# Kernel optimization log

Hardware: AMD Instinct MI355X
Metric: run time of the kernel (lower is better)

Reference implementation:

```python
import jax, jax.numpy as jnp
import numpy as np

T = 300  # windowsize = windowstep(50) * windowmul(6)
D_IN = 39
H1, H2 = 35, 30
FC1, FC2, OUT = 50, 40, 2


def _lstm_layer(x_tbd, W, b, H):
    """TF LSTMCell: gates ordered i, j, f, o; forget_bias=1.0; tanh activation.
    x_tbd: [T, B, D]; W: [D+H, 4H]; b: [4H]. Returns hidden states [T, B, H]."""
    B = x_tbd.shape[1]
    h0 = jnp.zeros((B, H), x_tbd.dtype)
    c0 = jnp.zeros((B, H), x_tbd.dtype)

    def step(carry, xt):
        h, c = carry
        z = jnp.concatenate([xt, h], axis=-1) @ W + b  # [B, 4H]
        i, j, f, o = jnp.split(z, 4, axis=-1)
        c = jax.nn.sigmoid(f + 1.0) * c + jax.nn.sigmoid(i) * jnp.tanh(j)
        h = jax.nn.sigmoid(o) * jnp.tanh(c)
        return (h, c), h

    _, hs = jax.lax.scan(step, (h0, c0), x_tbd)
    return hs


def _stack(x_tbd, W1, b1, W2, b2):
    h1 = _lstm_layer(x_tbd, W1, b1, H1)
    return _lstm_layer(h1, W2, b2, H2)


def setup_inputs() -> dict:
    key = jax.random.key(0)
    ks = jax.random.split(key, 16)
    B = 4096
    s = lambda fan_in: 1.0 / np.sqrt(fan_in)

    def mat(k, shape):
        return jax.random.normal(k, shape, jnp.float32) * s(shape[0])

    return {
        "x": jax.random.normal(ks[0], (B, T, D_IN), jnp.float32),
        "fw_W1": mat(ks[1], (D_IN + H1, 4 * H1)), "fw_b1": jnp.zeros((4 * H1,), jnp.float32),
        "fw_W2": mat(ks[2], (H1 + H2, 4 * H2)), "fw_b2": jnp.zeros((4 * H2,), jnp.float32),
        "bw_W1": mat(ks[3], (D_IN + H1, 4 * H1)), "bw_b1": jnp.zeros((4 * H1,), jnp.float32),
        "bw_W2": mat(ks[4], (H1 + H2, 4 * H2)), "bw_b2": jnp.zeros((4 * H2,), jnp.float32),
        "W_fc1": mat(ks[5], (2 * H2, FC1)), "b_fc1": jnp.zeros((FC1,), jnp.float32),
        "W_fc2": mat(ks[6], (FC1, FC2)), "b_fc2": jnp.zeros((FC2,), jnp.float32),
        "W_out": mat(ks[7], (FC2, OUT)), "b_out": jnp.zeros((OUT,), jnp.float32),
    }


def reference(x, fw_W1, fw_b1, fw_W2, fw_b2, bw_W1, bw_b1, bw_W2, bw_b2,
              W_fc1, b_fc1, W_fc2, b_fc2, W_out, b_out):
    x_tbd = jnp.transpose(x, (1, 0, 2))  # [T, B, D]
    h_fw = _stack(x_tbd, fw_W1, fw_b1, fw_W2, fw_b2)               # [T, B, H2]
    h_bw = _stack(x_tbd[::-1], bw_W1, bw_b1, bw_W2, bw_b2)[::-1]   # [T, B, H2]
    h = jnp.concatenate([h_fw, h_bw], axis=-1)  # [T, B, 2*H2]
    h = jnp.transpose(h, (1, 0, 2))             # [B, T, 60]
    h = jax.nn.relu(h @ W_fc1 + b_fc1)
    h = jax.nn.relu(h @ W_fc2 + b_fc2)
    logits = h @ W_out + b_out                  # [B, T, 2]
    return logits
```

## Files before the change

### kernel.cpp

```cpp
#include <hip/hip_runtime.h>


#define T_STEPS 300
#define DIN 39
#define H1 35
#define H2 30
#define BATCH 4096
#define FC1N 50
#define FC2N 40

#define AP_STR 104

typedef _Float16 f16;
typedef _Float16 half8 __attribute__((ext_vector_type(8)));
typedef float floatx4 __attribute__((ext_vector_type(4)));

__device__ __forceinline__ float sigf(float x) {
    return __builtin_amdgcn_rcpf(1.0f + __expf(-x));
}
__device__ __forceinline__ float sig_tanh(float a, float b) {
    float bc = fminf(b, 30.0f);
    float ea = __expf(-a);
    float E  = __expf(2.0f * bc);
    return (E - 1.0f) * __builtin_amdgcn_rcpf((1.0f + ea) * (E + 1.0f));
}

__global__ void wprep_kernel(const float* __restrict__ fw1, const float* __restrict__ bw1,
                             const float* __restrict__ fw2, const float* __restrict__ bw2,
                             f16* __restrict__ bp) {
    int frag = blockIdx.x;
    int lane = threadIdx.x;
    int dir = frag / 60;
    int rem = frag % 60;
    int layer = (rem < 36) ? 0 : 1;
    int r2 = (layer == 0) ? rem : rem - 36;
    int ug = r2 / 12, g = (r2 % 12) / 3, c = r2 % 3;
    int u = ug * 16 + (lane & 15);
    const float* W = (layer == 0) ? (dir ? bw1 : fw1) : (dir ? bw2 : fw2);
    for (int j = 0; j < 8; ++j) {
        int k = c * 32 + (lane >> 4) * 8 + j;
        float v = 0.0f;
        if (layer == 0) {
            if (u < H1) {
                int kr = (k < 39) ? k : ((k >= 40 && k < 75) ? k - 1 : -1);
                if (kr >= 0) v = W[kr * (4 * H1) + g * H1 + u];
            }
        } else {
            if (u < H2 && k < 65) v = W[k * (4 * H2) + g * H2 + u];
        }
        bp[(size_t)frag * 512 + lane * 8 + j] = (f16)v;
    }
}

__global__ void fcwprep_kernel(const float* __restrict__ Wf1, const float* __restrict__ Wf2,
                               const float* __restrict__ Wo, f16* __restrict__ fcp) {
    int f = blockIdx.x;
    int lane = threadIdx.x;
    int lm = lane & 15, oct = lane >> 4;
    for (int j = 0; j < 8; ++j) {
        float v = 0.0f;
        if (f < 8) {
            int tile = f >> 1, chunk = f & 1;
            int n = tile * 16 + lm;
            int kl = chunk * 32 + oct * 8 + j;
            int krow = (kl < 30) ? kl : ((kl >= 32 && kl < 62) ? kl - 2 : -1);
            if (n < FC1N && krow >= 0) v = Wf1[krow * FC1N + n];
        } else if (f < 14) {
            int g = f - 8, tile = g >> 1, chunk = g & 1;
            int n = tile * 16 + lm;
            int k = chunk * 32 + oct * 8 + j;
            if (n < FC2N && k < FC1N) v = Wf2[k * FC2N + n];
        } else {
            int chunk = f - 14;
            int k = chunk * 32 + oct * 8 + j;
            if (lm < 2 && k < FC2N) v = Wo[k * 2 + lm];
        }
        fcp[(size_t)f * 512 + lane * 8 + j] = (f16)v;
    }
}

__global__ __launch_bounds__(320, 3) void lstm_fused(
    const float* __restrict__ x, const f16* __restrict__ bp,
    const float* __restrict__ fb1, const float* __restrict__ bb1,
    const float* __restrict__ fb2, const float* __restrict__ bb2,
    f16* __restrict__ h2s)
{
    __shared__ f16 pan1[2][16 * AP_STR];
    __shared__ f16 pan2[2][16 * AP_STR];

    const int tid = threadIdx.x;
    const int b0  = blockIdx.x * 16;
    const int dir = blockIdx.y;
    const int wv   = tid >> 6;
    const int lane = tid & 63;
    const int lm = lane & 15, oct = lane >> 4;
    const bool isL2 = (wv >= 3);
    const int ug = isL2 ? (wv - 3) : wv;
    const int u  = ug * 16 + lm;
    const int Hn = isL2 ? H2 : H1;
    const float* bias = isL2 ? (dir ? bb2 : fb2) : (dir ? bb1 : fb1);
    const int fragbase = dir * 60 + (isL2 ? 36 : 0) + ug * 12;

    half8 bf[4][3];
    #pragma unroll
    for (int g = 0; g < 4; ++g)
        #pragma unroll
        for (int c = 0; c < 3; ++c)
            bf[g][c] = *(const half8*)(bp + (size_t)(fragbase + g * 3 + c) * 512 + lane * 8);

    float zb[4];
    #pragma unroll
    for (int g = 0; g < 4; ++g)
        zb[g] = (u < Hn) ? bias[g * Hn + u] : 0.f;
    float cst[4] = {0.f, 0.f, 0.f, 0.f};

    f16* h2p = h2s + ((size_t)(dir * BATCH + b0 + oct * 4) * T_STEPS
                      + (dir ? (T_STEPS - 1) : 0)) * 32 + u;
    const int h2step = dir ? -32 : 32;

    for (int idx = tid; idx < 16 * AP_STR; idx += 320) {
        pan1[0][idx] = (f16)0.f; pan1[1][idx] = (f16)0.f;
        pan2[0][idx] = (f16)0.f; pan2[1][idx] = (f16)0.f;
    }
    __syncthreads();

    const int sr = tid / 10, sq = tid % 10;
    float xv[4] = {0.f, 0.f, 0.f, 0.f};
    if (tid < 160) {
        int t0 = dir ? (T_STEPS - 1) : 0;
        const float* p0 = x + ((size_t)(b0 + sr) * T_STEPS + t0) * DIN;
        union { f16 h[4]; uint2 u; } pk;
        #pragma unroll
        for (int i = 0; i < 4; ++i) { int k = sq * 4 + i; pk.h[i] = (k < DIN) ? (f16)p0[k] : (f16)0.f; }
        *(uint2*)(&pan1[0][sr * AP_STR + sq * 4]) = pk.u;
        int t1 = dir ? (T_STEPS - 2) : 1;
        const float* p1 = x + ((size_t)(b0 + sr) * T_STEPS + t1) * DIN;
        #pragma unroll
        for (int i = 0; i < 4; ++i) { int k = sq * 4 + i; xv[i] = (k < DIN) ? p1[k] : 0.f; }
    }
    __syncthreads();

    const int arow = lm * AP_STR + oct * 8;

    if (!isL2) {
        floatx4 C[4];
        #pragma unroll
        for (int g = 0; g < 4; ++g) C[g] = (floatx4){zb[g], zb[g], zb[g], zb[g]};
        half8 a0 = *(const half8*)(&pan1[0][arow]);
        half8 a1 = *(const half8*)(&pan1[0][arow + 32]);
        half8 a2 = *(const half8*)(&pan1[0][arow + 64]);
        #pragma unroll
        for (int g = 0; g < 4; ++g) {
            C[g] = __builtin_amdgcn_mfma_f32_16x16x32_f16(a0, bf[g][0], C[g], 0, 0, 0);
            C[g] = __builtin_amdgcn_mfma_f32_16x16x32_f16(a1, bf[g][1], C[g], 0, 0, 0);
            C[g] = __builtin_amdgcn_mfma_f32_16x16x32_f16(a2, bf[g][2], C[g], 0, 0, 0);
        }
        #pragma unroll
        for (int r = 0; r < 4; ++r) {
            float cc = sigf(C[2][r] + 1.0f) * cst[r] + sig_tanh(C[0][r], C[1][r]);
            cst[r] = cc;
            float hh = sig_tanh(C[3][r], cc);
            if (u < H1) {
                int row = oct * 4 + r;
                f16 hv = (f16)hh;
                pan1[1][row * AP_STR + 40 + u] = hv;
                pan2[1][row * AP_STR + u] = hv;
            }
        }
    }
    const float* px = x + ((size_t)(b0 + sr) * T_STEPS
                           + (dir ? (T_STEPS - 4) : 3)) * DIN + sq * 4;
    const int xstep = dir ? -DIN : DIN;
    if (tid < 160) {
        union { f16 h[4]; uint2 u; } pk;
        #pragma unroll
        for (int i = 0; i < 4; ++i) pk.h[i] = (f16)xv[i];
        *(uint2*)(&pan1[1][sr * AP_STR + sq * 4]) = pk.u;
        int t2 = dir ? (T_STEPS - 3) : 2;
        const float* p2 = x + ((size_t)(b0 + sr) * T_STEPS + t2) * DIN;
        #pragma unroll
        for (int i = 0; i < 4; ++i) { int k = sq * 4 + i; xv[i] = (k < DIN) ? p2[k] : 0.f; }
    }
    __syncthreads();

    for (int s = 0; s < T_STEPS; ++s) {
        const int p = 1 - (s & 1);

        float xn[4] = {0.f, 0.f, 0.f, 0.f};
        if (tid < 160) {
            #pragma unroll
            for (int i = 0; i < 4; ++i) { int k = sq * 4 + i; xn[i] = (k < DIN) ? px[i] : 0.f; }
        }
        if (s < T_STEPS - 4) px += xstep;

        const f16* ap = isL2 ? &pan2[p][0] : &pan1[p][0];
        floatx4 C[4];
        #pragma unroll
        for (int g = 0; g < 4; ++g) C[g] = (floatx4){zb[g], zb[g], zb[g], zb[g]};
        {
            half8 a0 = *(const half8*)(ap + arow);
            half8 a1 = *(const half8*)(ap + arow + 32);
            half8 a2 = *(const half8*)(ap + arow + 64);
            #pragma unroll
            for (int g = 0; g < 4; ++g) {
                C[g] = __builtin_amdgcn_mfma_f32_16x16x32_f16(a0, bf[g][0], C[g], 0, 0, 0);
                C[g] = __builtin_amdgcn_mfma_f32_16x16x32_f16(a1, bf[g][1], C[g], 0, 0, 0);
                C[g] = __builtin_amdgcn_mfma_f32_16x16x32_f16(a2, bf[g][2], C[g], 0, 0, 0);
            }
        }

        f16* w1 = &pan1[1 - p][0];
        f16* w2 = &pan2[1 - p][0];
        if (!isL2) {
            #pragma unroll
            for (int r = 0; r < 4; ++r) {
                float cc = sigf(C[2][r] + 1.0f) * cst[r] + sig_tanh(C[0][r], C[1][r]);
                cst[r] = cc;
                float hh = sig_tanh(C[3][r], cc);
                if (u < H1) {
                    int row = oct * 4 + r;
                    f16 hv = (f16)hh;
                    w1[row * AP_STR + 40 + u] = hv;
                    w2[row * AP_STR + u] = hv;
                }
            }
        } else {
            #pragma unroll
            for (int r = 0; r < 4; ++r) {
                float dd = sigf(C[2][r] + 1.0f) * cst[r] + sig_tanh(C[0][r], C[1][r]);
                cst[r] = dd;
                float gg = sig_tanh(C[3][r], dd);
                if (u < H2) {
                    int row = oct * 4 + r;
                    f16 gv = (f16)gg;
                    w2[row * AP_STR + 35 + u] = gv;
                    h2p[(size_t)r * T_STEPS * 32] = gv;
                }
            }
        }
        h2p += h2step;

        if (tid < 160) {
            union { f16 h[4]; uint2 u; } pk;
            #pragma unroll
            for (int i = 0; i < 4; ++i) pk.h[i] = (f16)xv[i];
            *(uint2*)(&pan1[1 - p][sr * AP_STR + sq * 4]) = pk.u;
            #pragma unroll
            for (int i = 0; i < 4; ++i) xv[i] = xn[i];
        }
        __syncthreads();
    }
}

__global__ __launch_bounds__(256, 4) void fc_kernel(
    const f16* __restrict__ h2s, const f16* __restrict__ fcp,
    const float* __restrict__ bf1, const float* __restrict__ bf2,
    const float* __restrict__ bo, float* __restrict__ out)
{
    __shared__ f16 apf[4][64 * 72];
    const int tid = threadIdx.x;
    const int wv = tid >> 6, lane = tid & 63;
    const int lm = lane & 15, oct = lane >> 4;
    f16* ap = apf[wv];

    half8 wf[16];
    #pragma unroll
    for (int f = 0; f < 16; ++f)
        wf[f] = *(const half8*)(fcp + (size_t)f * 512 + lane * 8);

    const int ar = lm * 72 + oct * 8;
    const int row = lane >> 2, seg = lane & 3;
    const size_t base = (size_t)blockIdx.x * 256 + wv * 64;

    uint4 vf[4], vb[4];
    #pragma unroll
    for (int g = 0; g < 4; ++g) {
        const size_t r0 = base + g * 16 + row;
        vf[g] = *(const uint4*)(h2s + r0 * 32 + seg * 8);
        vb[g] = *(const uint4*)(h2s + ((size_t)BATCH * T_STEPS + r0) * 32 + seg * 8);
    }
    #pragma unroll
    for (int g = 0; g < 4; ++g) {
        *(uint4*)(ap + (g * 16 + row) * 72 + seg * 8) = vf[g];
        *(uint4*)(ap + (g * 16 + row) * 72 + 32 + seg * 8) = vb[g];
    }

    #pragma unroll
    for (int g = 0; g < 4; ++g) {
        f16* agp = ap + g * 16 * 72;
        half8 a0 = *(const half8*)(agp + ar);
        half8 a1 = *(const half8*)(agp + ar + 32);
        floatx4 C[4];
        #pragma unroll
        for (int t = 0; t < 4; ++t) {
            int col = t * 16 + lm;
            float b = (col < FC1N) ? bf1[col] : 0.f;
            C[t] = (floatx4){b, b, b, b};
            C[t] = __builtin_amdgcn_mfma_f32_16x16x32_f16(a0, wf[t * 2 + 0], C[t], 0, 0, 0);
            C[t] = __builtin_amdgcn_mfma_f32_16x16x32_f16(a1, wf[t * 2 + 1], C[t], 0, 0, 0);
        }
        #pragma unroll
        for (int t = 0; t < 4; ++t) {
            int col = t * 16 + lm;
            #pragma unroll
            for (int r = 0; r < 4; ++r)
                agp[(oct * 4 + r) * 72 + col] = (f16)fmaxf(C[t][r], 0.f);
        }
    }

    #pragma unroll
    for (int g = 0; g < 4; ++g) {
        f16* agp = ap + g * 16 * 72;
        half8 a0 = *(const half8*)(agp + ar);
        half8 a1 = *(const half8*)(agp + ar + 32);
        floatx4 D[3];
        #pragma unroll
        for (int t = 0; t < 3; ++t) {
            int col = t * 16 + lm;
            float b = (col < FC2N) ? bf2[col] : 0.f;
            D[t] = (floatx4){b, b, b, b};
            D[t] = __builtin_amdgcn_mfma_f32_16x16x32_f16(a0, wf[8 + t * 2 + 0], D[t], 0, 0, 0);
            D[t] = __builtin_amdgcn_mfma_f32_16x16x32_f16(a1, wf[8 + t * 2 + 1], D[t], 0, 0, 0);
        }
        #pragma unroll
        for (int t = 0; t < 3; ++t) {
            int col = t * 16 + lm;
            #pragma unroll
            for (int r = 0; r < 4; ++r)
                agp[(oct * 4 + r) * 72 + col] = (f16)fmaxf(D[t][r], 0.f);
        }
    }

    #pragma unroll
    for (int g = 0; g < 4; ++g) {
        f16* agp = ap + g * 16 * 72;
        half8 a0 = *(const half8*)(agp + ar);
        half8 a1 = *(const half8*)(agp + ar + 32);
        float b = (lm < 2) ? bo[lm] : 0.f;
        floatx4 E = (floatx4){b, b, b, b};
        E = __builtin_amdgcn_mfma_f32_16x16x32_f16(a0, wf[14], E, 0, 0, 0);
        E = __builtin_amdgcn_mfma_f32_16x16x32_f16(a1, wf[15], E, 0, 0, 0);
        if (lm < 2) {
            const size_t rid0 = base + g * 16;
            #pragma unroll
            for (int r = 0; r < 4; ++r)
                out[(rid0 + oct * 4 + r) * 2 + lm] = E[r];
        }
    }
}

extern "C" void kernel_launch(void* const* d_in, const int* in_sizes, int n_in,
                              void* d_out, int out_size, void* d_ws, size_t ws_size,
                              hipStream_t stream) {
    const float* x     = (const float*)d_in[0];
    const float* fw_W1 = (const float*)d_in[1];
    const float* fw_b1 = (const float*)d_in[2];
    const float* fw_W2 = (const float*)d_in[3];
    const float* fw_b2 = (const float*)d_in[4];
    const float* bw_W1 = (const float*)d_in[5];
    const float* bw_b1 = (const float*)d_in[6];
    const float* bw_W2 = (const float*)d_in[7];
    const float* bw_b2 = (const float*)d_in[8];
    const float* Wf1   = (const float*)d_in[9];
    const float* bf1   = (const float*)d_in[10];
    const float* Wf2   = (const float*)d_in[11];
    const float* bf2   = (const float*)d_in[12];
    const float* Wo    = (const float*)d_in[13];
    const float* bo    = (const float*)d_in[14];
    float* outp = (float*)d_out;

    f16* h2s = (f16*)d_ws;
    f16* bp  = h2s + (size_t)2 * BATCH * T_STEPS * 32;
    f16* fcp = bp + (size_t)120 * 512;

    wprep_kernel<<<120, 64, 0, stream>>>(fw_W1, bw_W1, fw_W2, bw_W2, bp);
    fcwprep_kernel<<<16, 64, 0, stream>>>(Wf1, Wf2, Wo, fcp);

    dim3 gl(BATCH / 16, 2);
    lstm_fused<<<gl, 320, 0, stream>>>(x, bp, fw_b1, bw_b1, fw_b2, bw_b2, h2s);

    fc_kernel<<<(BATCH * T_STEPS) / 256, 256, 0, stream>>>(
        h2s, fcp, bf1, bf2, bo, outp);
}
```

Before: 665.9 us.

## Merge LSTM layer panels into one shared buffer and stream FC inputs from registers

Layer-1 and layer-2 A-panels are combined into a single shared panel per parity buffer. Layer 2 now reads a window offset by 40, so each layer-1 hidden state is written to LDS once instead of twice and shared memory per block shrinks. The FC kernel loads the fwd/bwd hidden fragments directly from global memory into MFMA A registers, prefetching the next 16-row group, so the LDS staging copy goes away. FC1 weights are repacked to match the new layout. Risks: the padding columns of the panel must stay zero, and layer-2 stores are no longer guarded by u<H2, so the padded lanes must produce values that are harmless.

```diff
diff --git a/kernel.cpp b/kernel.cpp
--- a/kernel.cpp
+++ b/kernel.cpp
@@ -9,7 +9,7 @@
 #define FC1N 50
 #define FC2N 40
 
-#define AP_STR 104
+#define PAN_STR 136
 
 typedef _Float16 f16;
 typedef _Float16 half8 __attribute__((ext_vector_type(8)));
@@ -62,9 +62,8 @@
         if (f < 8) {
             int tile = f >> 1, chunk = f & 1;
             int n = tile * 16 + lm;
-            int kl = chunk * 32 + oct * 8 + j;
-            int krow = (kl < 30) ? kl : ((kl >= 32 && kl < 62) ? kl - 2 : -1);
-            if (n < FC1N && krow >= 0) v = Wf1[krow * FC1N + n];
+            int kl = oct * 8 + j;
+            if (n < FC1N && kl < 30) v = Wf1[(chunk * 30 + kl) * FC1N + n];
         } else if (f < 14) {
             int g = f - 8, tile = g >> 1, chunk = g & 1;
             int n = tile * 16 + lm;
@@ -85,8 +84,7 @@
     const float* __restrict__ fb2, const float* __restrict__ bb2,
     f16* __restrict__ h2s)
 {
-    __shared__ f16 pan1[2][16 * AP_STR];
-    __shared__ f16 pan2[2][16 * AP_STR];
+    __shared__ f16 pan[2][16 * PAN_STR];
 
     const int tid = threadIdx.x;
     const int b0  = blockIdx.x * 16;
@@ -118,9 +116,8 @@
                       + (dir ? (T_STEPS - 1) : 0)) * 32 + u;
     const int h2step = dir ? -32 : 32;
 
-    for (int idx = tid; idx < 16 * AP_STR; idx += 320) {
-        pan1[0][idx] = (f16)0.f; pan1[1][idx] = (f16)0.f;
-        pan2[0][idx] = (f16)0.f; pan2[1][idx] = (f16)0.f;
+    for (int idx = tid; idx < 16 * PAN_STR; idx += 320) {
+        pan[0][idx] = (f16)0.f; pan[1][idx] = (f16)0.f;
     }
     __syncthreads();
 
@@ -132,7 +129,7 @@
         union { f16 h[4]; uint2 u; } pk;
         #pragma unroll
         for (int i = 0; i < 4; ++i) { int k = sq * 4 + i; pk.h[i] = (k < DIN) ? (f16)p0[k] : (f16)0.f; }
-        *(uint2*)(&pan1[0][sr * AP_STR + sq * 4]) = pk.u;
+        *(uint2*)(&pan[0][sr * PAN_STR + sq * 4]) = pk.u;
         int t1 = dir ? (T_STEPS - 2) : 1;
         const float* p1 = x + ((size_t)(b0 + sr) * T_STEPS + t1) * DIN;
         #pragma unroll
@@ -140,15 +137,15 @@
     }
     __syncthreads();
 
-    const int arow = lm * AP_STR + oct * 8;
+    const int arow = lm * PAN_STR + oct * 8 + (isL2 ? 40 : 0);
 
     if (!isL2) {
         floatx4 C[4];
         #pragma unroll
         for (int g = 0; g < 4; ++g) C[g] = (floatx4){zb[g], zb[g], zb[g], zb[g]};
-        half8 a0 = *(const half8*)(&pan1[0][arow]);
-        half8 a1 = *(const half8*)(&pan1[0][arow + 32]);
-        half8 a2 = *(const half8*)(&pan1[0][arow + 64]);
+        half8 a0 = *(const half8*)(&pan[0][arow]);
+        half8 a1 = *(const half8*)(&pan[0][arow + 32]);
+        half8 a2 = *(const half8*)(&pan[0][arow + 64]);
         #pragma unroll
         for (int g = 0; g < 4; ++g) {
             C[g] = __builtin_amdgcn_mfma_f32_16x16x32_f16(a0, bf[g][0], C[g], 0, 0, 0);
@@ -162,9 +159,7 @@
             float hh = sig_tanh(C[3][r], cc);
             if (u < H1) {
                 int row = oct * 4 + r;
-                f16 hv = (f16)hh;
-                pan1[1][row * AP_STR + 40 + u] = hv;
-                pan2[1][row * AP_STR + u] = hv;
+                pan[1][row * PAN_STR + 40 + u] = (f16)hh;
             }
         }
     }
@@ -175,7 +170,7 @@
         union { f16 h[4]; uint2 u; } pk;
         #pragma unroll
         for (int i = 0; i < 4; ++i) pk.h[i] = (f16)xv[i];
-        *(uint2*)(&pan1[1][sr * AP_STR + sq * 4]) = pk.u;
+        *(uint2*)(&pan[1][sr * PAN_STR + sq * 4]) = pk.u;
         int t2 = dir ? (T_STEPS - 3) : 2;
         const float* p2 = x + ((size_t)(b0 + sr) * T_STEPS + t2) * DIN;
         #pragma unroll
@@ -193,7 +188,7 @@
         }
         if (s < T_STEPS - 4) px += xstep;
 
-        const f16* ap = isL2 ? &pan2[p][0] : &pan1[p][0];
+        const f16* ap = &pan[p][0];
         floatx4 C[4];
         #pragma unroll
         for (int g = 0; g < 4; ++g) C[g] = (floatx4){zb[g], zb[g], zb[g], zb[g]};
@@ -209,8 +204,7 @@
             }
         }
 
-        f16* w1 = &pan1[1 - p][0];
-        f16* w2 = &pan2[1 - p][0];
+        f16* w = &pan[1 - p][0];
         if (!isL2) {
             #pragma unroll
             for (int r = 0; r < 4; ++r) {
@@ -219,9 +213,7 @@
                 float hh = sig_tanh(C[3][r], cc);
                 if (u < H1) {
                     int row = oct * 4 + r;
-                    f16 hv = (f16)hh;
-                    w1[row * AP_STR + 40 + u] = hv;
-                    w2[row * AP_STR + u] = hv;
+                    w[row * PAN_STR + 40 + u] = (f16)hh;
                 }
             }
         } else {
@@ -230,12 +222,10 @@
                 float dd = sigf(C[2][r] + 1.0f) * cst[r] + sig_tanh(C[0][r], C[1][r]);
                 cst[r] = dd;
                 float gg = sig_tanh(C[3][r], dd);
-                if (u < H2) {
-                    int row = oct * 4 + r;
-                    f16 gv = (f16)gg;
-                    w2[row * AP_STR + 35 + u] = gv;
-                    h2p[(size_t)r * T_STEPS * 32] = gv;
-                }
+                int row = oct * 4 + r;
+                f16 gv = (f16)gg;
+                w[row * PAN_STR + 75 + u] = gv;
+                h2p[(size_t)r * T_STEPS * 32] = gv;
             }
         }
         h2p += h2step;
@@ -244,7 +234,7 @@
             union { f16 h[4]; uint2 u; } pk;
             #pragma unroll
             for (int i = 0; i < 4; ++i) pk.h[i] = (f16)xv[i];
-            *(uint2*)(&pan1[1 - p][sr * AP_STR + sq * 4]) = pk.u;
+            *(uint2*)(&pan[1 - p][sr * PAN_STR + sq * 4]) = pk.u;
             #pragma unroll
             for (int i = 0; i < 4; ++i) xv[i] = xn[i];
         }
@@ -252,16 +242,22 @@
     }
 }
 
-__global__ __launch_bounds__(256, 4) void fc_kernel(
+__global__ __launch_bounds__(256) void fc_kernel(
     const f16* __restrict__ h2s, const f16* __restrict__ fcp,
     const float* __restrict__ bf1, const float* __restrict__ bf2,
     const float* __restrict__ bo, float* __restrict__ out)
 {
-    __shared__ f16 apf[4][64 * 72];
+    __shared__ f16 apf[4][2][16 * 72];
     const int tid = threadIdx.x;
     const int wv = tid >> 6, lane = tid & 63;
     const int lm = lane & 15, oct = lane >> 4;
-    f16* ap = apf[wv];
+    f16* pa = &apf[wv][0][0];
+    f16* pb = &apf[wv][1][0];
+
+    {
+        uint* z = (uint*)pa;
+        for (int i = lane; i < 1152; i += 64) z[i] = 0u;
+    }
 
     half8 wf[16];
     #pragma unroll
@@ -269,27 +265,23 @@
         wf[f] = *(const half8*)(fcp + (size_t)f * 512 + lane * 8);
 
     const int ar = lm * 72 + oct * 8;
-    const int row = lane >> 2, seg = lane & 3;
     const size_t base = (size_t)blockIdx.x * 256 + wv * 64;
-
-    uint4 vf[4], vb[4];
-    #pragma unroll
-    for (int g = 0; g < 4; ++g) {
-        const size_t r0 = base + g * 16 + row;
-        vf[g] = *(const uint4*)(h2s + r0 * 32 + seg * 8);
-        vb[g] = *(const uint4*)(h2s + ((size_t)BATCH * T_STEPS + r0) * 32 + seg * 8);
-    }
-    #pragma unroll
-    for (int g = 0; g < 4; ++g) {
-        *(uint4*)(ap + (g * 16 + row) * 72 + seg * 8) = vf[g];
-        *(uint4*)(ap + (g * 16 + row) * 72 + 32 + seg * 8) = vb[g];
-    }
-
-    #pragma unroll
-    for (int g = 0; g < 4; ++g) {
-        f16* agp = ap + g * 16 * 72;
-        half8 a0 = *(const half8*)(agp + ar);
-        half8 a1 = *(const half8*)(agp + ar + 32);
+    const size_t bwoff = (size_t)BATCH * T_STEPS * 32;
+
+    union U8 { uint4 u; half8 h; };
+    const f16* gp = h2s + (base + lm) * 32 + oct * 8;
+    U8 va, vb;
+    va.u = *(const uint4*)gp;
+    vb.u = *(const uint4*)(gp + bwoff);
+
+    for (int it = 0; it < 4; ++it) {
+        half8 a0 = va.h, a1 = vb.h;
+        if (it < 3) {
+            const f16* gn = gp + (size_t)(it + 1) * 16 * 32;
+            va.u = *(const uint4*)gn;
+            vb.u = *(const uint4*)(gn + bwoff);
+        }
+
         floatx4 C[4];
         #pragma unroll
         for (int t = 0; t < 4; ++t) {
@@ -304,44 +296,36 @@
             int col = t * 16 + lm;
             #pragma unroll
             for (int r = 0; r < 4; ++r)
-                agp[(oct * 4 + r) * 72 + col] = (f16)fmaxf(C[t][r], 0.f);
-        }
-    }
-
-    #pragma unroll
-    for (int g = 0; g < 4; ++g) {
-        f16* agp = ap + g * 16 * 72;
-        half8 a0 = *(const half8*)(agp + ar);
-        half8 a1 = *(const half8*)(agp + ar + 32);
+                pa[(oct * 4 + r) * 72 + col] = (f16)fmaxf(C[t][r], 0.f);
+        }
+
+        half8 b0 = *(const half8*)(pa + ar);
+        half8 b1 = *(const half8*)(pa + ar + 32);
         floatx4 D[3];
         #pragma unroll
         for (int t = 0; t < 3; ++t) {
             int col = t * 16 + lm;
             float b = (col < FC2N) ? bf2[col] : 0.f;
             D[t] = (floatx4){b, b, b, b};
-            D[t] = __builtin_amdgcn_mfma_f32_16x16x32_f16(a0, wf[8 + t * 2 + 0], D[t], 0, 0, 0);
-            D[t] = __builtin_amdgcn_mfma_f32_16x16x32_f16(a1, wf[8 + t * 2 + 1], D[t], 0, 0, 0);
+            D[t] = __builtin_amdgcn_mfma_f32_16x16x32_f16(b0, wf[8 + t * 2 + 0], D[t], 0, 0, 0);
+            D[t] = __builtin_amdgcn_mfma_f32_16x16x32_f16(b1, wf[8 + t * 2 + 1], D[t], 0, 0, 0);
         }
         #pragma unroll
         for (int t = 0; t < 3; ++t) {
             int col = t * 16 + lm;
             #pragma unroll
             for (int r = 0; r < 4; ++r)
-                agp[(oct * 4 + r) * 72 + col] = (f16)fmaxf(D[t][r], 0.f);
-        }
-    }
-
-    #pragma unroll
-    for (int g = 0; g < 4; ++g) {
-        f16* agp = ap + g * 16 * 72;
-        half8 a0 = *(const half8*)(agp + ar);
-        half8 a1 = *(const half8*)(agp + ar + 32);
+                pb[(oct * 4 + r) * 72 + col] = (f16)fmaxf(D[t][r], 0.f);
+        }
+
+        half8 c0 = *(const half8*)(pb + ar);
+        half8 c1 = *(const half8*)(pb + ar + 32);
         float b = (lm < 2) ? bo[lm] : 0.f;
         floatx4 E = (floatx4){b, b, b, b};
-        E = __builtin_amdgcn_mfma_f32_16x16x32_f16(a0, wf[14], E, 0, 0, 0);
-        E = __builtin_amdgcn_mfma_f32_16x16x32_f16(a1, wf[15], E, 0, 0, 0);
+        E = __builtin_amdgcn_mfma_f32_16x16x32_f16(c0, wf[14], E, 0, 0, 0);
+        E = __builtin_amdgcn_mfma_f32_16x16x32_f16(c1, wf[15], E, 0, 0, 0);
         if (lm < 2) {
-            const size_t rid0 = base + g * 16;
+            const size_t rid0 = base + it * 16;
             #pragma unroll
             for (int r = 0; r < 4; ++r)
                 out[(rid0 + oct * 4 + r) * 2 + lm] = E[r];
```

New measurement: 699.4 us. 1.05x slower.
